# Kernel optimization log

Hardware: AMD Instinct MI355X
Metric: run time of the kernel (lower is better)

The kernel has to match this reference:

```python
import jax, jax.numpy as jnp
import numpy as np

N = 8_000_000
LOG_HALF = -0.6931471805599453  # log(1/2)

DATASET_MAP = {0: 0, 1: 0, 2: 0, 3: 0, 4: 1, 5: 1, 6: 1, 7: 1}
LOSS_RECIPE = [(0, 4, 4), (0, 6, 4), (1, 5, 5), (1, 6, 5), (2, 4, 4), (2, 5, 5), (2, 6, 6), (2, 7, 7),
               (4, 0, 4), (4, 2, 4), (5, 1, 5), (5, 2, 5), (6, 2, 6), (7, 2, 7)]
NEG_LOSS_RECIPE = [(0, 4, 1), (0, 4, 2), (0, 6, 1), (0, 6, 2), (1, 5, 0), (1, 5, 2), (1, 6, 0), (1, 6, 2),
                   (2, 4, 1), (2, 4, 2), (2, 5, 0), (2, 5, 2), (4, 0, 1), (4, 0, 2), (4, 2, 1), (4, 2, 2),
                   (5, 1, 0), (5, 1, 2), (5, 2, 0), (5, 2, 2), (2, 7, 2), (7, 2, 2)]


def log1mexp(x):
    """Numerically stable log(1 - exp(x)) for x < 0 (grad-safe where)."""
    big = x > LOG_HALF
    xb = jnp.where(big, x, -1.0)   # branch-safe operands
    xs = jnp.where(big, -1.0, x)
    return jnp.where(big, jnp.log(-jnp.expm1(xb)), jnp.log1p(-jnp.exp(xs)))


def create_probabilities(v1, v2):
    l1, l2 = log1mexp(v1), log1mexp(v2)
    return [v1 + l2, l1 + v2, v1 + v2, l1 + l2]  # PC, CP, CR, NR


def setup_inputs() -> dict:
    key = jax.random.key(0)
    ks = jax.random.split(key, 9)
    def vol(k):
        u = jax.random.uniform(k, (N, 2), dtype=jnp.float32, minval=1e-6, maxval=1.0 - 1e-6)
        return jnp.log(u)  # strictly negative log-probabilities
    names = ["vol_AB", "vol_BA", "vol_BC", "vol_CB", "vol_AC", "vol_CA"]
    inp = {n: vol(k) for n, k in zip(names, ks[:6])}
    inp["xy_rel_id"] = jax.random.randint(ks[6], (N, 2), 0, 2)
    inp["yz_rel_id"] = jax.random.randint(ks[7], (N, 2), 0, 2)
    inp["xz_rel_id"] = jax.random.randint(ks[8], (N, 2), 0, 2)
    return inp


def reference(vol_AB, vol_BA, vol_BC, vol_CB, vol_AC, vol_CA, xy_rel_id, yz_rel_id, xz_rel_id):
    pAB = create_probabilities(vol_AB, vol_BA)
    pBC = create_probabilities(vol_BC, vol_CB)
    pAC = create_probabilities(vol_AC, vol_CA)
    loss = jnp.float32(0.0)
    for xy, yz, xz in LOSS_RECIPE:
        f1, f2, f3 = DATASET_MAP[xy], DATASET_MAP[yz], DATASET_MAP[xz]
        term = pAB[xy % 4][:, f1] + pBC[yz % 4][:, f2] - pAC[xz % 4][:, f3]
        loss = loss + jnp.maximum(0.0, term).sum()
    for xy, yz, xz in NEG_LOSS_RECIPE:
        f1, f2, f3 = DATASET_MAP[xy], DATASET_MAP[yz], DATASET_MAP[xz]
        term = pAB[xy % 4][:, f1] + pBC[yz % 4][:, f2] - log1mexp(pAC[xz % 4][:, f3])
        loss = loss + jnp.maximum(0.0, term).sum()
    return loss
```

## Files before the change

kernel.cpp:

```cpp
#include <hip/hip_runtime.h>


#define LOG2E 1.4426950408889634f
#define LN2   0.6931471805599453f

__device__ __forceinline__ float fexp2(float x) { return __builtin_amdgcn_exp2f(x); }
__device__ __forceinline__ float flog2(float x) { return __builtin_amdgcn_logf(x); }
__device__ __forceinline__ float relu_(float x) { return fmaxf(x, 0.0f); }

__device__ __forceinline__ float row_loss_l2(
    float a0, float a1, float b0, float b1,
    float c0, float c1, float d0, float d1,
    float e0, float e1, float f0, float f1)
{
    float a0s = a0 * LOG2E, a1s = a1 * LOG2E;
    float b0s = b0 * LOG2E, b1s = b1 * LOG2E;
    float c0s = c0 * LOG2E, c1s = c1 * LOG2E;
    float d0s = d0 * LOG2E, d1s = d1 * LOG2E;
    float e0s = e0 * LOG2E, e1s = e1 * LOG2E;
    float f0s = f0 * LOG2E, f1s = f1 * LOG2E;

    float ua0 = fexp2(a0s), ub0 = fexp2(b0s), uc0 = fexp2(c0s), ud0 = fexp2(d0s);
    float ue0 = fexp2(e0s), uf0 = fexp2(f0s);
    float ua1 = fexp2(a1s), ub1 = fexp2(b1s), uc1 = fexp2(c1s), ud1 = fexp2(d1s);
    float ue1 = fexp2(e1s), uf1 = fexp2(f1s);

    float wa0 = 1.0f - ua0, wb0 = 1.0f - ub0, wc0 = 1.0f - uc0, wd0 = 1.0f - ud0;
    float we0 = 1.0f - ue0, wf0 = 1.0f - uf0;
    float wa1 = 1.0f - ua1, wb1 = 1.0f - ub1, wc1 = 1.0f - uc1, wd1 = 1.0f - ud1;
    float we1 = 1.0f - ue1, wf1 = 1.0f - uf1;

    float la0 = flog2(wa0), lb0 = flog2(wb0), lc0 = flog2(wc0), ld0 = flog2(wd0);
    float la1 = flog2(wa1), lb1 = flog2(wb1), lc1 = flog2(wc1), ld1 = flog2(wd1);
    float le1 = flog2(we1), lf1 = flog2(wf1);

    float LAC0 = flog2(fmaf(-ue0, wf0, 1.0f));
    float LAC1 = flog2(fmaf(-we0, uf0, 1.0f));
    float LAC2 = flog2(fmaf(-ue0, uf0, 1.0f));

    float AB00 = a0s + lb0, AB10 = la0 + b0s, AB20 = a0s + b0s;
    float AB01 = a1s + lb1, AB11 = la1 + b1s, AB21 = a1s + b1s, AB31 = la1 + lb1;
    float BC00 = c0s + ld0, BC10 = lc0 + d0s, BC20 = c0s + d0s;
    float BC01 = c1s + ld1, BC11 = lc1 + d1s, BC21 = c1s + d1s, BC31 = lc1 + ld1;
    float AC01 = e1s + lf1, AC11 = le1 + f1s, AC21 = e1s + f1s, AC31 = le1 + lf1;

    float s1  = AB00 + BC01, s2  = AB00 + BC21, s3  = AB10 + BC11, s4  = AB10 + BC21;
    float s5  = AB20 + BC01, s6  = AB20 + BC11, s7  = AB20 + BC21, s8  = AB20 + BC31;
    float s9  = AB01 + BC00, s10 = AB01 + BC20, s11 = AB11 + BC10, s12 = AB11 + BC20;
    float s13 = AB21 + BC20, s14 = AB31 + BC20;

    float p = 0.0f, q = 0.0f;
    p += relu_(s1 - AC01) + relu_(s2 - AC01) + relu_(s3 - AC11) + relu_(s4 - AC11);
    q += relu_(s5 - AC01) + relu_(s6 - AC11) + relu_(s7 - AC21) + relu_(s8 - AC31);
    p += relu_(s9 - AC01) + relu_(s10 - AC01) + relu_(s11 - AC11) + relu_(s12 - AC11);
    q += relu_(s13 - AC21) + relu_(s14 - AC31);
    p += relu_(s1 - LAC1) + relu_(s1 - LAC2) + relu_(s2 - LAC1) + relu_(s2 - LAC2);
    q += relu_(s3 - LAC0) + relu_(s3 - LAC2) + relu_(s4 - LAC0) + relu_(s4 - LAC2);
    p += relu_(s5 - LAC1) + relu_(s5 - LAC2) + relu_(s6 - LAC0) + relu_(s6 - LAC2);
    q += relu_(s9 - LAC1) + relu_(s9 - LAC2) + relu_(s10 - LAC1) + relu_(s10 - LAC2);
    p += relu_(s11 - LAC0) + relu_(s11 - LAC2) + relu_(s12 - LAC0) + relu_(s12 - LAC2);
    q += relu_(s8 - LAC2) + relu_(s14 - LAC2);
    return p + q;
}

struct Seg2 {
    float2 ab, ba, bc, cb, ac, ca;
};

__device__ __forceinline__ float row_loss_seg(const Seg2& s)
{
    return row_loss_l2(s.ab.x, s.ab.y, s.ba.x, s.ba.y, s.bc.x, s.bc.y,
                       s.cb.x, s.cb.y, s.ac.x, s.ac.y, s.ca.x, s.ca.y);
}

__global__ __launch_bounds__(256)
__attribute__((amdgpu_waves_per_eu(6, 8)))
void box_loss_kernel(
    const float* __restrict__ AB, const float* __restrict__ BA,
    const float* __restrict__ BC, const float* __restrict__ CB,
    const float* __restrict__ AC, const float* __restrict__ CA,
    float* __restrict__ out, unsigned nElems)
{
    const unsigned nE = nElems;
    const unsigned T = (unsigned)gridDim.x * blockDim.x * 2u;
    unsigned t = ((unsigned)blockIdx.x * blockDim.x + threadIdx.x) * 2u;

    const unsigned nT = (nE + T - 1u) / T;
    const int pairs = (int)((nT + 1u) / 2u);

    #define LOAD_SEG(dst, msk, base)                        \
        do {                                                \
            bool v_ = ((base) + 2u) <= nE;                  \
            unsigned a_ = v_ ? (base) : 0u;                 \
            (msk) = v_ ? 1.0f : 0.0f;                       \
            (dst).ab = *(const float2*)(AB + a_);           \
            (dst).ba = *(const float2*)(BA + a_);           \
            (dst).bc = *(const float2*)(BC + a_);           \
            (dst).cb = *(const float2*)(CB + a_);           \
            (dst).ac = *(const float2*)(AC + a_);           \
            (dst).ca = *(const float2*)(CA + a_);           \
        } while (0)

    Seg2 X, Y;
    float mX, mY;

    LOAD_SEG(X, mX, t); t += T;
    LOAD_SEG(Y, mY, t); t += T;
    __builtin_amdgcn_sched_barrier(0);

    float acc = 0.0f;
    for (int r = 0; r < pairs - 1; ++r) {
        acc += mX * row_loss_seg(X);
        LOAD_SEG(X, mX, t); t += T;
        __builtin_amdgcn_sched_barrier(0);

        acc += mY * row_loss_seg(Y);
        LOAD_SEG(Y, mY, t); t += T;
        __builtin_amdgcn_sched_barrier(0);
    }
    acc += mX * row_loss_seg(X);
    acc += mY * row_loss_seg(Y);
    #undef LOAD_SEG

    acc *= LN2;

    #pragma unroll
    for (int off = 32; off > 0; off >>= 1)
        acc += __shfl_down(acc, off, 64);

    __shared__ float wsum[4];
    const int lane = threadIdx.x & 63;
    const int wid  = threadIdx.x >> 6;
    if (lane == 0) wsum[wid] = acc;
    __syncthreads();
    if (threadIdx.x == 0) {
        float s = wsum[0] + wsum[1] + wsum[2] + wsum[3];
        atomicAdd(out, s);
    }
}

extern "C" void kernel_launch(void* const* d_in, const int* in_sizes, int n_in,
                              void* d_out, int out_size, void* d_ws, size_t ws_size,
                              hipStream_t stream) {
    const float* AB = (const float*)d_in[0];
    const float* BA = (const float*)d_in[1];
    const float* BC = (const float*)d_in[2];
    const float* CB = (const float*)d_in[3];
    const float* AC = (const float*)d_in[4];
    const float* CA = (const float*)d_in[5];

    const unsigned nElems = (unsigned)in_sizes[0];
    const int block = 256;
    const int grid = 2048;

    hipMemsetAsync(d_out, 0, (size_t)out_size * sizeof(float), stream);
    box_loss_kernel<<<grid, block, 0, stream>>>(AB, BA, BC, CB, AC, CA,
                                                (float*)d_out, nElems);
}
```

Measured before the change: 512.5 us.

## Stage input tiles into LDS via async global_load_lds with triple buffering

Replaces the register double-buffered float2 loads with direct global-to-LDS 16-byte async loads into a three-stage ring of shared-memory tiles. Each thread now processes four elements (two rows) per tile, and the grid shrinks from 2048 to 512 blocks with 72 KB of dynamic LDS per block. The aim is to keep more memory traffic in flight and free registers for the transcendental-heavy compute. In exchange it adds per-iteration block barriers and vmcnt waits, and the large LDS footprint limits how many blocks can be resident.

Result: faster. 442.2 us (-13.7%).

```diff
diff --git a/kernel.cpp b/kernel.cpp
--- a/kernel.cpp
+++ b/kernel.cpp
@@ -7,6 +7,14 @@
 __device__ __forceinline__ float fexp2(float x) { return __builtin_amdgcn_exp2f(x); }
 __device__ __forceinline__ float flog2(float x) { return __builtin_amdgcn_logf(x); }
 __device__ __forceinline__ float relu_(float x) { return fmaxf(x, 0.0f); }
+
+__device__ __forceinline__ void stage16(const float* g, float* l)
+{
+    __builtin_amdgcn_global_load_lds(
+        (const __attribute__((address_space(1))) void*)g,
+        (__attribute__((address_space(3))) void*)l,
+        16, 0, 0);
+}
 
 __device__ __forceinline__ float row_loss_l2(
     float a0, float a1, float b0, float b1,
@@ -63,64 +71,78 @@
     return p + q;
 }
 
-struct Seg2 {
-    float2 ab, ba, bc, cb, ac, ca;
-};
 
-__device__ __forceinline__ float row_loss_seg(const Seg2& s)
-{
-    return row_loss_l2(s.ab.x, s.ab.y, s.ba.x, s.ba.y, s.bc.x, s.bc.y,
-                       s.cb.x, s.cb.y, s.ac.x, s.ac.y, s.ca.x, s.ca.y);
-}
-
-__global__ __launch_bounds__(256)
-__attribute__((amdgpu_waves_per_eu(6, 8)))
-void box_loss_kernel(
+__global__ __launch_bounds__(256) void box_loss_kernel(
     const float* __restrict__ AB, const float* __restrict__ BA,
     const float* __restrict__ BC, const float* __restrict__ CB,
     const float* __restrict__ AC, const float* __restrict__ CA,
     float* __restrict__ out, unsigned nElems)
 {
+    extern __shared__ __align__(16) float lds[];
+
     const unsigned nE = nElems;
-    const unsigned T = (unsigned)gridDim.x * blockDim.x * 2u;
-    unsigned t = ((unsigned)blockIdx.x * blockDim.x + threadIdx.x) * 2u;
+    const int tid  = threadIdx.x;
+    const int wid  = tid >> 6;
+    const int lane = tid & 63;
+    const int G    = gridDim.x;
+    const int bid  = blockIdx.x;
+    const unsigned tOff = (unsigned)tid * 4u;
 
-    const unsigned nT = (nE + T - 1u) / T;
-    const int pairs = (int)((nT + 1u) / 2u);
+    const int nT = (int)((nE + 1023u) / 1024u);
+    int myCount  = (nT - bid + G - 1) / G;
+    if (myCount < 1) myCount = 1;
+    const int lastI = myCount - 1;
 
-    #define LOAD_SEG(dst, msk, base)                        \
-        do {                                                \
-            bool v_ = ((base) + 2u) <= nE;                  \
-            unsigned a_ = v_ ? (base) : 0u;                 \
-            (msk) = v_ ? 1.0f : 0.0f;                       \
-            (dst).ab = *(const float2*)(AB + a_);           \
-            (dst).ba = *(const float2*)(BA + a_);           \
-            (dst).bc = *(const float2*)(BC + a_);           \
-            (dst).cb = *(const float2*)(CB + a_);           \
-            (dst).ac = *(const float2*)(AC + a_);           \
-            (dst).ca = *(const float2*)(CA + a_);           \
+    #define ISSUE(buf, tile)                                            \
+        do {                                                            \
+            unsigned e_ = (unsigned)(tile) * 1024u + tOff;              \
+            unsigned a_ = (e_ + 4u <= nE) ? e_ : 0u;                    \
+            float* lb_ = lds + (((buf) * 24) + wid) * 256;              \
+            stage16(AB + a_, lb_ + 0 * 1024);                           \
+            stage16(BA + a_, lb_ + 1 * 1024);                           \
+            stage16(BC + a_, lb_ + 2 * 1024);                           \
+            stage16(CB + a_, lb_ + 3 * 1024);                           \
+            stage16(AC + a_, lb_ + 4 * 1024);                           \
+            stage16(CA + a_, lb_ + 5 * 1024);                           \
         } while (0)
 
-    Seg2 X, Y;
-    float mX, mY;
-
-    LOAD_SEG(X, mX, t); t += T;
-    LOAD_SEG(Y, mY, t); t += T;
+    ISSUE(0, bid);
+    ISSUE(1, (1 <= lastI) ? (bid + G) : bid);
     __builtin_amdgcn_sched_barrier(0);
 
     float acc = 0.0f;
-    for (int r = 0; r < pairs - 1; ++r) {
-        acc += mX * row_loss_seg(X);
-        LOAD_SEG(X, mX, t); t += T;
+    for (int i = 0; i < myCount; ++i) {
+        asm volatile("s_waitcnt vmcnt(6)" ::: "memory");
+        __builtin_amdgcn_s_barrier();
         __builtin_amdgcn_sched_barrier(0);
 
-        acc += mY * row_loss_seg(Y);
-        LOAD_SEG(Y, mY, t); t += T;
+        {
+            int j = i + 2;
+            int tj = (j <= lastI) ? (bid + j * G) : (bid + lastI * G);
+            ISSUE(j % 3, tj);
+        }
         __builtin_amdgcn_sched_barrier(0);
+
+        {
+            const float* lb = lds + ((i % 3) * 24 + wid) * 256 + lane * 4;
+            float4 vab = *(const float4*)(lb + 0 * 1024);
+            float4 vba = *(const float4*)(lb + 1 * 1024);
+            float4 vbc = *(const float4*)(lb + 2 * 1024);
+            float4 vcb = *(const float4*)(lb + 3 * 1024);
+            float4 vac = *(const float4*)(lb + 4 * 1024);
+            float4 vca = *(const float4*)(lb + 5 * 1024);
+
+            unsigned e = (unsigned)(bid + i * G) * 1024u + tOff;
+            float m = (e + 4u <= nE) ? 1.0f : 0.0f;
+
+            acc += m * (row_loss_l2(vab.x, vab.y, vba.x, vba.y, vbc.x, vbc.y,
+                                    vcb.x, vcb.y, vac.x, vac.y, vca.x, vca.y)
+                      + row_loss_l2(vab.z, vab.w, vba.z, vba.w, vbc.z, vbc.w,
+                                    vcb.z, vcb.w, vac.z, vac.w, vca.z, vca.w));
+        }
     }
-    acc += mX * row_loss_seg(X);
-    acc += mY * row_loss_seg(Y);
-    #undef LOAD_SEG
+    #undef ISSUE
+    asm volatile("s_waitcnt vmcnt(0)" ::: "memory");
 
     acc *= LN2;
 
@@ -129,11 +151,9 @@
         acc += __shfl_down(acc, off, 64);
 
     __shared__ float wsum[4];
-    const int lane = threadIdx.x & 63;
-    const int wid  = threadIdx.x >> 6;
     if (lane == 0) wsum[wid] = acc;
     __syncthreads();
-    if (threadIdx.x == 0) {
+    if (tid == 0) {
         float s = wsum[0] + wsum[1] + wsum[2] + wsum[3];
         atomicAdd(out, s);
     }
@@ -151,9 +171,10 @@
 
     const unsigned nElems = (unsigned)in_sizes[0];
     const int block = 256;
-    const int grid = 2048;
+    const int grid = 512;
+    const size_t ldsBytes = 3u * 6u * 4u * 256u * sizeof(float);
 
     hipMemsetAsync(d_out, 0, (size_t)out_size * sizeof(float), stream);
-    box_loss_kernel<<<grid, block, 0, stream>>>(AB, BA, BC, CB, AC, CA,
-                                                (float*)d_out, nElems);
+    box_loss_kernel<<<grid, block, ldsBytes, stream>>>(AB, BA, BC, CB, AC, CA,
+                                                       (float*)d_out, nElems);
 }
```
